# Kernel tuning notes

Hardware: AMD Instinct MI355X
Metric: run time of the kernel (lower is better)

Reference implementation:

```python
import jax, jax.numpy as jnp
import numpy as np

EPS = 1e-7  # keras backend epsilon
B, D_IN, H, L, DEPTH = 16384, 784, 512, 32, 2

def _lrelu(x):
    return jax.nn.leaky_relu(x, 0.3)  # tf.keras LeakyReLU default alpha

def _router(h, W1, b1, W2, b2, W3, b3):
    h = _lrelu(h @ W1 + b1)
    h = _lrelu(h @ W2 + b2)
    return jax.nn.sigmoid((h @ W3 + b3)[:, 0])

def setup_inputs():
    key = jax.random.key(0)
    ks = jax.random.split(key, 20)
    s = 0.02
    n = lambda k, sh: jax.random.normal(k, sh, jnp.float32) * s
    return {
        'x': jax.random.uniform(ks[0], (B, D_IN), jnp.float32),
        'enc_W0': n(ks[1], (D_IN, H)), 'enc_b0': jnp.zeros((H,), jnp.float32),
        'enc_W': n(ks[2], (3, H, H)), 'enc_b': jnp.zeros((3, H), jnp.float32),
        'dense_Wmu': n(ks[3], (7, H, L)), 'dense_bmu': jnp.zeros((7, L), jnp.float32),
        'dense_Wsig': n(ks[4], (7, H, L)), 'dense_bsig': jnp.zeros((7, L), jnp.float32),
        'trans_Wh': n(ks[5], (6, L, H)), 'trans_bh': jnp.zeros((6, H), jnp.float32),
        'trans_Wmu': n(ks[6], (6, H, L)), 'trans_bmu': jnp.zeros((6, L), jnp.float32),
        'trans_Wsig': n(ks[7], (6, H, L)), 'trans_bsig': jnp.zeros((6, L), jnp.float32),
        'routp_W1': n(ks[8], (3, L, H)), 'routp_b1': jnp.zeros((3, H), jnp.float32),
        'routp_W2': n(ks[9], (3, H, H)), 'routp_b2': jnp.zeros((3, H), jnp.float32),
        'routp_W3': n(ks[10], (3, H, 1)), 'routp_b3': jnp.zeros((3, 1), jnp.float32),
        'routq_W1': n(ks[11], (3, H, H)), 'routq_b1': jnp.zeros((3, H), jnp.float32),
        'routq_W2': n(ks[12], (3, H, H)), 'routq_b2': jnp.zeros((3, H), jnp.float32),
        'routq_W3': n(ks[13], (3, H, 1)), 'routq_b3': jnp.zeros((3, 1), jnp.float32),
        'dec_W1': n(ks[14], (4, L, H)), 'dec_b1': jnp.zeros((4, H), jnp.float32),
        'dec_W2': n(ks[15], (4, H, D_IN)), 'dec_b2': jnp.zeros((4, D_IN), jnp.float32),
    }

def reference(x, enc_W0, enc_b0, enc_W, enc_b,
              dense_Wmu, dense_bmu, dense_Wsig, dense_bsig,
              trans_Wh, trans_bh, trans_Wmu, trans_bmu, trans_Wsig, trans_bsig,
              routp_W1, routp_b1, routp_W2, routp_b2, routp_W3, routp_b3,
              routq_W1, routq_b1, routq_W2, routq_b2, routq_W3, routq_b3,
              dec_W1, dec_b1, dec_W2, dec_b2):
    Bn = x.shape[0]
    # bottom-up encoder chain; encoders collects layers i >= len - (depth+1) = 1
    d = _lrelu(x @ enc_W0 + enc_b0)
    encoders = []
    for i in range(3):
        d = _lrelu(d @ enc_W[i] + enc_b[i])
        encoders.append(d)
    depth_of = [0, 1, 1, 2, 2, 2, 2]  # BFS depth of the 7 tree nodes
    probs = {0: jnp.ones((Bn,), x.dtype)}
    zs = {}
    kl_nodes_tot = jnp.zeros((Bn,), x.dtype)
    kl_dec_tot = jnp.zeros((Bn,), x.dtype)
    kl_root = None
    leaves_prob, recons = [], []
    base = jax.random.key(1)
    for k in range(7):
        dl = depth_of[k]
        d = encoders[DEPTH - dl]
        mu_q_hat = d @ dense_Wmu[k] + dense_bmu[k]
        sig_q_hat = jax.nn.softplus(d @ dense_Wsig[k] + dense_bsig[k])
        if k == 0:
            mu_p = jnp.zeros_like(mu_q_hat)
            sig_p = jnp.ones_like(sig_q_hat)
            mu_q, sig_q = mu_q_hat, sig_q_hat
        else:
            zp = zs[(k - 1) // 2]
            h = _lrelu(zp @ trans_Wh[k - 1] + trans_bh[k - 1])
            mu_p = h @ trans_Wmu[k - 1] + trans_bmu[k - 1]
            sig_p = jax.nn.softplus(h @ trans_Wsig[k - 1] + trans_bsig[k - 1])
            # compute_posterior: precision-weighted fusion
            sig_q = 1.0 / (1.0 / sig_q_hat + 1.0 / sig_p)
            mu_q = sig_q * (mu_q_hat / sig_q_hat + mu_p / sig_p)
        vq = sig_q + EPS
        vp = sig_p + EPS
        # KL(N(mu_q, vq) || N(mu_p, vp)) for diag Gaussians (scale = sqrt(sigma+eps))
        kl = 0.5 * jnp.sum(vq / vp + (mu_q - mu_p) ** 2 / vp - 1.0 + jnp.log(vp / vq), axis=1)
        kl_node = jnp.clip(probs[k] * kl, -1.0, 1000.0)
        if k == 0:
            kl_root = kl_node
        else:
            kl_nodes_tot = kl_nodes_tot + kl_node
        eps_n = jax.random.normal(jax.random.fold_in(base, k), mu_q.shape, x.dtype)
        z = mu_q + jnp.sqrt(vq) * eps_n  # reparameterized sample
        zs[k] = z
        if k < 3:  # internal node: routing
            pl = _router(z, routp_W1[k], routp_b1[k], routp_W2[k], routp_b2[k], routp_W3[k], routp_b3[k])
            plq = _router(d, routq_W1[k], routq_b1[k], routq_W2[k], routq_b2[k], routq_W3[k], routq_b3[k])
            kl_dec = plq * jnp.log(EPS + plq / (pl + EPS)) + (1.0 - plq) * jnp.log(EPS + (1.0 - plq) / (1.0 - pl + EPS))
            kl_dec_tot = kl_dec_tot + probs[k] * kl_dec
            probs[2 * k + 1] = probs[k] * plq
            probs[2 * k + 2] = probs[k] * (1.0 - plq)
        else:  # leaf: decode
            leaves_prob.append(probs[k])
            h = _lrelu(z @ dec_W1[k - 3] + dec_b1[k - 3])
            recons.append(jax.nn.sigmoid(h @ dec_W2[k - 3] + dec_b2[k - 3]))
    rec_losses = jnp.zeros((Bn,), x.dtype)
    for p, r in zip(leaves_prob, recons):
        bce = -jnp.sum(x * jnp.log(r + EPS) + (1.0 - x) * jnp.log(1.0 - r + EPS), axis=1)
        rec_losses = rec_losses + p * bce
    # elbo_samples, per-sample total loss (shape [B])
    return kl_nodes_tot + kl_dec_tot + kl_root + rec_losses
```

## Files before the change

### kernel.cpp

```cpp
#include <hip/hip_runtime.h>
#include <cstdint>
#include <cstddef>

#define B_ROWS 16384
#define DIN 784
#define HD 512
#define LD 32

typedef __attribute__((ext_vector_type(8))) short short8;
typedef __attribute__((ext_vector_type(4))) float f32x4;
typedef __attribute__((ext_vector_type(4))) unsigned short us4;

struct I4 { int x, y, z, w; };
__device__ inline int i4get(I4 v, int z) { return z == 0 ? v.x : z == 1 ? v.y : z == 2 ? v.z : v.w; }

__device__ inline unsigned short f2bf(float v) {
  union { float f; unsigned u; } x; x.f = v;
  unsigned r = x.u + 0x7fffu + ((x.u >> 16) & 1u);
  return (unsigned short)(r >> 16);
}

__host__ __device__ inline void threefry2x32(uint32_t k0, uint32_t k1,
                                             uint32_t x0, uint32_t x1,
                                             uint32_t& o0, uint32_t& o1) {
  uint32_t ks2 = k0 ^ k1 ^ 0x1BD11BDAu;
#define TF_ROT(x, d) (((x) << (d)) | ((x) >> (32 - (d))))
#define TF_R(r) { x0 += x1; x1 = TF_ROT(x1, r); x1 ^= x0; }
  x0 += k0; x1 += k1;
  TF_R(13) TF_R(15) TF_R(26) TF_R(6)
  x0 += k1; x1 += ks2 + 1u;
  TF_R(17) TF_R(29) TF_R(16) TF_R(24)
  x0 += ks2; x1 += k0 + 2u;
  TF_R(13) TF_R(15) TF_R(26) TF_R(6)
  x0 += k0; x1 += k1 + 3u;
  TF_R(17) TF_R(29) TF_R(16) TF_R(24)
  x0 += k1; x1 += ks2 + 4u;
  TF_R(13) TF_R(15) TF_R(26) TF_R(6)
  x0 += ks2; x1 += k0 + 5u;
  o0 = x0; o1 = x1;
#undef TF_R
#undef TF_ROT
}

__device__ inline float erfinv_f(float x) {
  float w = -log1pf(-x * x);
  float p;
  if (w < 5.0f) {
    w -= 2.5f;
    p = 2.81022636e-08f;
    p = fmaf(p, w, 3.43273939e-07f);
    p = fmaf(p, w, -3.5233877e-06f);
    p = fmaf(p, w, -4.39150654e-06f);
    p = fmaf(p, w, 0.00021858087f);
    p = fmaf(p, w, -0.00125372503f);
    p = fmaf(p, w, -0.00417768164f);
    p = fmaf(p, w, 0.246640727f);
    p = fmaf(p, w, 1.50140941f);
  } else {
    w = sqrtf(w) - 3.0f;
    p = -0.000200214257f;
    p = fmaf(p, w, 0.000100950558f);
    p = fmaf(p, w, 0.00134934322f);
    p = fmaf(p, w, -0.00367342844f);
    p = fmaf(p, w, 0.00573950773f);
    p = fmaf(p, w, -0.0076224613f);
    p = fmaf(p, w, 0.00943887047f);
    p = fmaf(p, w, 1.00167406f);
    p = fmaf(p, w, 2.83297682f);
  }
  return p * x;
}

__device__ inline float jax_normal_elem(uint32_t ka, uint32_t kb, uint32_t idx) {
  uint32_t b1, b2;
  threefry2x32(ka, kb, 0u, idx, b1, b2);
  uint32_t bits = b1 ^ b2;
  uint32_t fb = (bits >> 9) | 0x3f800000u;
  float f = __uint_as_float(fb) - 1.0f;
  const float lo = -0.99999994f;
  float u = f * 2.0f + lo;
  u = fmaxf(u, lo);
  return 1.41421356f * erfinv_f(u);
}

struct WJob {
  unsigned short pi;
  unsigned src_off, dst_off, start;
  short K, N, Np, Kp;
};
struct WJobs { WJob j[56]; unsigned total; };

constexpr WJobs make_jobs() {
  WJobs W{};
  int idx = 0; unsigned start = 0; unsigned d = 0;
  auto add = [&](int pi, unsigned so, int K, int N, int Np, int Kp, unsigned doff) {
    W.j[idx].pi = (unsigned short)pi; W.j[idx].src_off = so; W.j[idx].dst_off = doff;
    W.j[idx].start = start; W.j[idx].K = (short)K; W.j[idx].N = (short)N;
    W.j[idx].Np = (short)Np; W.j[idx].Kp = (short)Kp;
    start += (unsigned)(Np * Kp); ++idx;
  };
  add(0, 0, 784, 512, 512, 800, d); d += 512 * 800;
  for (int i = 0; i < 3; ++i) { add(1, i * 262144u, 512, 512, 512, 512, d); d += 262144; }
  for (int k = 0; k < 7; ++k) { add(2, k * 16384u, 512, 32, 32, 512, d);
                                add(3, k * 16384u, 512, 32, 32, 512, d + 16384); d += 32768; }
  for (int i = 0; i < 6; ++i) { add(4, i * 16384u, 32, 512, 512, 32, d); d += 16384; }
  for (int i = 0; i < 6; ++i) { add(5, i * 16384u, 512, 32, 32, 512, d);
                                add(6, i * 16384u, 512, 32, 32, 512, d + 16384); d += 32768; }
  for (int k = 0; k < 3; ++k) { add(7, k * 16384u, 32, 512, 512, 32, d); d += 16384; }
  for (int k = 0; k < 3; ++k) { add(8, k * 262144u, 512, 512, 512, 512, d); d += 262144; }
  for (int k = 0; k < 3; ++k) { add(9, k * 262144u, 512, 512, 512, 512, d); d += 262144; }
  for (int k = 0; k < 3; ++k) { add(10, k * 262144u, 512, 512, 512, 512, d); d += 262144; }
  for (int i = 0; i < 4; ++i) { add(11, i * 16384u, 32, 512, 512, 32, d); d += 16384; }
  for (int i = 0; i < 4; ++i) { add(12, i * 401408u, 512, 784, 896, 512, d); d += 458752; }
  W.total = start;
  return W;
}
__device__ constexpr WJobs g_jobs = make_jobs();

struct TileTable { unsigned ts[57]; };
constexpr TileTable make_tiles() {
  TileTable T{}; WJobs J = make_jobs();
  unsigned acc = 0;
  for (int i = 0; i < 56; ++i) {
    T.ts[i] = acc;
    acc += (unsigned)(J.j[i].Np / 32) * (unsigned)(J.j[i].Kp / 32);
  }
  T.ts[56] = acc;
  return T;
}
__device__ constexpr TileTable g_tiles = make_tiles();

#define OFF_ENC0T 0u
#define OFF_ENCT 409600u
#define OFF_DENSE 1196032u
#define OFF_TWH 1425408u
#define OFF_TMS 1523712u
#define OFF_RP1 1720320u
#define OFF_RP2 1769472u
#define OFF_RQ1 2555904u
#define OFF_RQ2 3342336u
#define OFF_DC1 4128768u
#define OFF_DC2 4194304u
#define ARENA_ELEMS 6029312u

struct WSrcs { const float* p[13]; };

__global__ void wconv_k(WSrcs srcs, unsigned short* __restrict__ arena) {
  __shared__ unsigned short tile[32][34];
  unsigned bid = blockIdx.x;
  int jo = 0;
#pragma unroll 1
  while (jo + 1 < 56 && g_tiles.ts[jo + 1] <= bid) ++jo;
  const WJob J = g_jobs.j[jo];
  unsigned t = bid - g_tiles.ts[jo];
  unsigned ktiles = (unsigned)J.Kp / 32u;
  unsigned n0 = (t / ktiles) * 32u, k0 = (t % ktiles) * 32u;
  int ty = threadIdx.x >> 3, tx4 = (threadIdx.x & 7) * 4;
  float v0 = 0, v1 = 0, v2 = 0, v3 = 0;
  int kk = (int)k0 + ty;
  if (kk < J.K) {
    const float* sp = srcs.p[J.pi] + J.src_off + (size_t)kk * J.N + n0 + tx4;
    int nb = (int)(n0 + tx4);
    if (nb + 3 < J.N) {
      float4 v = *reinterpret_cast<const float4*>(sp);
      v0 = v.x; v1 = v.y; v2 = v.z; v3 = v.w;
    } else {
      if (nb + 0 < J.N) v0 = sp[0];
      if (nb + 1 < J.N) v1 = sp[1];
      if (nb + 2 < J.N) v2 = sp[2];
      if (nb + 3 < J.N) v3 = sp[3];
    }
  }
  tile[tx4 + 0][ty] = f2bf(v0);
  tile[tx4 + 1][ty] = f2bf(v1);
  tile[tx4 + 2][ty] = f2bf(v2);
  tile[tx4 + 3][ty] = f2bf(v3);
  __syncthreads();
  us4 w;
  w.x = tile[ty][tx4 + 0]; w.y = tile[ty][tx4 + 1];
  w.z = tile[ty][tx4 + 2]; w.w = tile[ty][tx4 + 3];
  *reinterpret_cast<us4*>(&arena[J.dst_off + (size_t)(n0 + ty) * J.Kp + k0 + tx4]) = w;
}

__global__ void xconv_k(const float* __restrict__ x, unsigned short* __restrict__ xb) {
  unsigned g = blockIdx.x * 256u + threadIdx.x;
  unsigned r = g / 200u, c4 = g % 200u;
  unsigned c = c4 * 4u;
  float v0 = 0, v1 = 0, v2 = 0, v3 = 0;
  if (c + 3 < 784u) {
    float4 v = *reinterpret_cast<const float4*>(x + (size_t)r * 784u + c);
    v0 = v.x; v1 = v.y; v2 = v.z; v3 = v.w;
  } else {
    if (c + 0 < 784u) v0 = x[(size_t)r * 784u + c + 0];
    if (c + 1 < 784u) v1 = x[(size_t)r * 784u + c + 1];
    if (c + 2 < 784u) v2 = x[(size_t)r * 784u + c + 2];
    if (c + 3 < 784u) v3 = x[(size_t)r * 784u + c + 3];
  }
  us4 w; w.x = f2bf(v0); w.y = f2bf(v1); w.z = f2bf(v2); w.w = f2bf(v3);
  *reinterpret_cast<us4*>(&xb[(size_t)r * 800u + c]) = w;
}

template <int BN, int ACT, typename OT>
__global__ void mgemm_k(const unsigned short* __restrict__ A, int sA,
                        const unsigned short* __restrict__ Wt,
                        const float* __restrict__ b1, const float* __restrict__ b2,
                        OT* __restrict__ C, int sC, int Nreal, int K,
                        I4 zAo, I4 zWo, I4 zCo, int zB1, int zB2,
                        const float* __restrict__ xx) {
  constexpr int BM = 128, BK = 32;
  constexpr int WN = BN / 2;
  constexpr int NF = WN / 16;
  __shared__ unsigned short As[BM][BK];
  __shared__ unsigned short Bs[BN][BK];
  __shared__ float sums[BM][2];
  const int z = blockIdx.z;
  A += i4get(zAo, z);
  Wt += i4get(zWo, z);
  C += i4get(zCo, z);
  b1 += (size_t)z * zB1;
  if (ACT == 3 || ACT == 4) { if (b2) b2 += (size_t)z * zB2; }

  const int tid = threadIdx.x;
  const int lane = tid & 63;
  const int wid = tid >> 6;
  const int wr = wid >> 1, wc = wid & 1;
  const int bm = blockIdx.x * BM;
  const int bn = blockIdx.y * BN;

  f32x4 acc[4][NF];
#pragma unroll
  for (int m = 0; m < 4; ++m)
#pragma unroll
    for (int n = 0; n < NF; ++n) acc[m][n] = (f32x4){0.f, 0.f, 0.f, 0.f};

  const int lr = lane >> 2;
  const int lk = (lane & 3) * 8;

  for (int k0 = 0; k0 < K; k0 += BK) {
#pragma unroll
    for (int cc = 0; cc < 2; ++cc) {
      int c = wid * 2 + cc;
      const unsigned short* g = A + (size_t)(bm + c * 16 + lr) * sA + k0 + lk;
      __builtin_amdgcn_global_load_lds(
          (const __attribute__((address_space(1))) void*)g,
          (__attribute__((address_space(3))) void*)(&As[c * 16][0]), 16, 0, 0);
    }
    constexpr int CB = BN / 16;
#pragma unroll
    for (int cc = 0; cc < CB / 4; ++cc) {
      int c = wid * (CB / 4) + cc;
      const unsigned short* g = Wt + (size_t)(bn + c * 16 + lr) * K + k0 + lk;
      __builtin_amdgcn_global_load_lds(
          (const __attribute__((address_space(1))) void*)g,
          (__attribute__((address_space(3))) void*)(&Bs[c * 16][0]), 16, 0, 0);
    }
    __syncthreads();

    short8 aF[4], bF[NF];
    const int ar = wr * 64 + (lane & 15);
    const int ac = (lane >> 4) * 8;
#pragma unroll
    for (int m = 0; m < 4; ++m)
      aF[m] = *reinterpret_cast<const short8*>(&As[ar + m * 16][ac]);
    const int br = wc * WN + (lane & 15);
#pragma unroll
    for (int n = 0; n < NF; ++n)
      bF[n] = *reinterpret_cast<const short8*>(&Bs[br + n * 16][ac]);
#pragma unroll
    for (int m = 0; m < 4; ++m)
#pragma unroll
      for (int n = 0; n < NF; ++n)
        acc[m][n] = __builtin_amdgcn_mfma_f32_16x16x32_bf16(aF[m], bF[n], acc[m][n], 0, 0, 0);
    __syncthreads();
  }

  if constexpr (ACT == 4 || ACT == 5) {
    const int row0 = bm + wr * 64 + (lane >> 4) * 4;
#pragma unroll
    for (int m = 0; m < 4; ++m) {
#pragma unroll
      for (int r = 0; r < 4; ++r) {
        float s = 0.0f;
        int grow = row0 + m * 16 + r;
#pragma unroll
        for (int n = 0; n < NF; ++n) {
          int col = bn + wc * WN + n * 16 + (lane & 15);
          float v = acc[m][n][r];
          if constexpr (ACT == 4) {
            v += b1[col];
            v = (v >= 0.0f) ? v : 0.3f * v;
            s += v * b2[col];
          } else {
            if (col < Nreal) {
              v += b1[col];
              float sg = 1.0f / (1.0f + expf(-v));
              float xv = xx[(size_t)grow * Nreal + col];
              s += xv * logf(sg + 1e-7f) + (1.0f - xv) * logf(1.0f - sg + 1e-7f);
            }
          }
        }
#pragma unroll
        for (int msk = 1; msk < 16; msk <<= 1) s += __shfl_xor(s, msk, 64);
        if ((lane & 15) == 0) sums[wr * 64 + m * 16 + (lane >> 4) * 4 + r][wc] = s;
      }
    }
    __syncthreads();
    if (tid < BM) {
      float* Cf = (float*)C;
      Cf[(size_t)(bm + tid) * sC + blockIdx.y] = sums[tid][0] + sums[tid][1];
    }
  } else {
#pragma unroll
    for (int m = 0; m < 4; ++m) {
      int row = bm + wr * 64 + m * 16 + (lane >> 4) * 4;
#pragma unroll
      for (int n = 0; n < NF; ++n) {
        int col = bn + wc * WN + n * 16 + (lane & 15);
        if (col < Nreal) {
#pragma unroll
          for (int r = 0; r < 4; ++r) {
            float v = acc[m][n][r];
            if constexpr (ACT == 3) {
              int nl = col >> 6, cin = col & 63;
              if (cin < 32) {
                v += b1[nl * 32 + cin];
              } else {
                v += b2[nl * 32 + (cin - 32)];
                v = fmaxf(v, 0.0f) + log1pf(expf(-fabsf(v)));
              }
            } else {
              v += b1[col];
              if (ACT == 1) v = (v >= 0.0f) ? v : 0.3f * v;
            }
            size_t oidx = (size_t)(row + r) * sC + col;
            if constexpr (sizeof(OT) == 2) C[oidx] = (OT)f2bf(v);
            else C[oidx] = (OT)v;
          }
        }
      }
    }
  }
}

struct Keys { uint32_t a[7]; uint32_t b[7]; };

__global__ void node_k(int kstart, Keys keys,
                       const float* __restrict__ musigAll,
                       const float* __restrict__ mupsigAll,
                       const float* __restrict__ probs,
                       unsigned short* __restrict__ zbuf,
                       float* __restrict__ contrib) {
  const int knode = kstart + blockIdx.y;
  const int row = blockIdx.x * 8 + (threadIdx.x >> 5);
  const int j = threadIdx.x & 31;
  const float* mq = musigAll + (size_t)row * 448 + 64 * knode;
  float mqh = mq[j], sqh = mq[32 + j];
  float mu_q, sig_q, mu_p, sig_p;
  if (knode == 0) {
    mu_p = 0.0f; sig_p = 1.0f; mu_q = mqh; sig_q = sqh;
  } else {
    const float* mp = mupsigAll + (size_t)row * 448 + 64 * knode;
    mu_p = mp[j]; sig_p = mp[32 + j];
    sig_q = 1.0f / (1.0f / sqh + 1.0f / sig_p);
    mu_q = sig_q * (mqh / sqh + mu_p / sig_p);
  }
  float vq = sig_q + 1e-7f, vp = sig_p + 1e-7f;
  float dm = mu_q - mu_p;
  float kj = vq / vp + dm * dm / vp - 1.0f + logf(vp / vq);
#pragma unroll
  for (int msk = 1; msk < 32; msk <<= 1) kj += __shfl_xor(kj, msk, 64);
  float e = jax_normal_elem(keys.a[knode], keys.b[knode], (uint32_t)(row * 32 + j));
  zbuf[(size_t)knode * B_ROWS * 32 + (size_t)row * 32 + j] = f2bf(mu_q + sqrtf(vq) * e);
  if (j == 0) {
    float p = (knode == 0) ? 1.0f : probs[(size_t)knode * B_ROWS + row];
    float kn = fminf(fmaxf(p * 0.5f * kj, -1.0f), 1000.0f);
    contrib[(size_t)knode * B_ROWS + row] = kn;
  }
}

__global__ void route_k(int kstart, const float* __restrict__ plp,
                        const float* __restrict__ plqp,
                        const float* __restrict__ rpb3, const float* __restrict__ rqb3,
                        float* __restrict__ probs, float* __restrict__ contrib) {
  const int k = kstart + blockIdx.y;
  const int row = blockIdx.x * 256 + threadIdx.x;
  const float* pp = plp + ((size_t)k * B_ROWS + row) * 4;
  const float* pq = plqp + ((size_t)k * B_ROWS + row) * 4;
  float sl = pp[0] + pp[1] + pp[2] + pp[3];
  float sq = pq[0] + pq[1] + pq[2] + pq[3];
  float pl = 1.0f / (1.0f + expf(-(sl + rpb3[k])));
  float plq = 1.0f / (1.0f + expf(-(sq + rqb3[k])));
  float p = (k == 0) ? 1.0f : probs[(size_t)k * B_ROWS + row];
  float kld = plq * logf(1e-7f + plq / (pl + 1e-7f)) +
              (1.0f - plq) * logf(1e-7f + (1.0f - plq) / (1.0f - pl + 1e-7f));
  contrib[(size_t)(7 + k) * B_ROWS + row] = p * kld;
  probs[(size_t)(2 * k + 1) * B_ROWS + row] = p * plq;
  probs[(size_t)(2 * k + 2) * B_ROWS + row] = p * (1.0f - plq);
}

__global__ void final_k(const float* __restrict__ contrib, const float* __restrict__ probs,
                        const float* __restrict__ pbce, float* __restrict__ out) {
  const int row = blockIdx.x * 256 + threadIdx.x;
  float s = 0.0f;
#pragma unroll
  for (int i = 0; i < 10; ++i) s += contrib[(size_t)i * B_ROWS + row];
#pragma unroll
  for (int l = 0; l < 4; ++l) {
    const float* pb = pbce + ((size_t)l * B_ROWS + row) * 7;
    float bs = 0.0f;
#pragma unroll
    for (int y = 0; y < 7; ++y) bs += pb[y];
    s += probs[(size_t)(3 + l) * B_ROWS + row] * (-bs);
  }
  out[row] = s;
}

extern "C" void kernel_launch(void* const* d_in, const int* in_sizes, int n_in,
                              void* d_out, int out_size, void* d_ws, size_t ws_size,
                              hipStream_t stream) {
  const float* x      = (const float*)d_in[0];
  const float* enc_W0 = (const float*)d_in[1];
  const float* enc_b0 = (const float*)d_in[2];
  const float* enc_W  = (const float*)d_in[3];
  const float* enc_b  = (const float*)d_in[4];
  const float* dWmu   = (const float*)d_in[5];
  const float* dbmu   = (const float*)d_in[6];
  const float* dWsig  = (const float*)d_in[7];
  const float* dbsig  = (const float*)d_in[8];
  const float* tWh    = (const float*)d_in[9];
  const float* tbh    = (const float*)d_in[10];
  const float* tWmu   = (const float*)d_in[11];
  const float* tbmu   = (const float*)d_in[12];
  const float* tWsig  = (const float*)d_in[13];
  const float* tbsig  = (const float*)d_in[14];
  const float* rpW1   = (const float*)d_in[15];
  const float* rpb1   = (const float*)d_in[16];
  const float* rpW2   = (const float*)d_in[17];
  const float* rpb2   = (const float*)d_in[18];
  const float* rpW3   = (const float*)d_in[19];
  const float* rpb3   = (const float*)d_in[20];
  const float* rqW1   = (const float*)d_in[21];
  const float* rqb1   = (const float*)d_in[22];
  const float* rqW2   = (const float*)d_in[23];
  const float* rqb2   = (const float*)d_in[24];
  const float* rqW3   = (const float*)d_in[25];
  const float* rqb3   = (const float*)d_in[26];
  const float* dcW1   = (const float*)d_in[27];
  const float* dcb1   = (const float*)d_in[28];
  const float* dcW2   = (const float*)d_in[29];
  const float* dcb2   = (const float*)d_in[30];
  float* out = (float*)d_out;
  (void)in_sizes; (void)n_in; (void)out_size; (void)ws_size;

  const size_t BR = B_ROWS;
  unsigned short* h = (unsigned short*)d_ws;
  unsigned short* bufH = h;
  unsigned short* encA = h + BR * 512;
  unsigned short* encB = h + BR * 1024;
  unsigned short* encC = h + BR * 1536;
  unsigned short* bufT = h + BR * 2048;
  unsigned short* zbuf = h + BR * 3072;
  unsigned short* arena = h + BR * 3296;
  size_t ho = BR * 3296 + ARENA_ELEMS;
  float* f = (float*)(h + ho);
  float* musigAll  = f;
  float* mupsigAll = f + BR * 448;
  float* probs     = f + BR * 896;
  float* plp       = f + BR * 903;
  float* plqp      = f + BR * 915;
  float* pbce      = f + BR * 927;
  float* contrib   = f + BR * 955;
  unsigned short* xb = (unsigned short*)f;

  const int offA = (int)(BR * 512);
  const int offC = (int)(BR * 1536);

  Keys keys;
  for (int k = 0; k < 7; ++k) threefry2x32(0u, 1u, 0u, (uint32_t)k, keys.a[k], keys.b[k]);

  const I4 Z0 = {0, 0, 0, 0};
  constexpr TileTable HT = make_tiles();

  xconv_k<<<dim3((B_ROWS * 200) / 256), 256, 0, stream>>>(x, xb);
  WSrcs srcs;
  srcs.p[0] = enc_W0; srcs.p[1] = enc_W; srcs.p[2] = dWmu; srcs.p[3] = dWsig;
  srcs.p[4] = tWh; srcs.p[5] = tWmu; srcs.p[6] = tWsig;
  srcs.p[7] = rpW1; srcs.p[8] = rpW2; srcs.p[9] = rqW1; srcs.p[10] = rqW2;
  srcs.p[11] = dcW1; srcs.p[12] = dcW2;
  wconv_k<<<dim3(HT.ts[56]), 256, 0, stream>>>(srcs, arena);

#define LAUNCH(BN, ACT, OT, A, sA, W, B1, B2, Cc, sC, Nr, K, gy, gz, zA, zW, zC, zb1, zb2, XX) \
  mgemm_k<BN, ACT, OT><<<dim3(B_ROWS / 128, gy, gz), 256, 0, stream>>>( \
      A, sA, W, B1, B2, Cc, sC, Nr, K, zA, zW, zC, zb1, zb2, XX)

  LAUNCH(128, 1, unsigned short, xb, 800, arena + OFF_ENC0T, enc_b0, nullptr,
         bufH, 512, 512, 800, 4, 1, Z0, Z0, Z0, 0, 0, nullptr);
  LAUNCH(128, 1, unsigned short, bufH, 512, arena + OFF_ENCT + 0u, enc_b + 0, nullptr,
         encA, 512, 512, 512, 4, 1, Z0, Z0, Z0, 0, 0, nullptr);
  LAUNCH(128, 3, float, encA, 512, arena + OFF_DENSE + 3u * 32768u, dbmu + 96, dbsig + 96,
         musigAll + 192, 448, 256, 512, 2, 1, Z0, Z0, Z0, 0, 0, nullptr);
  LAUNCH(128, 1, unsigned short, encA, 512, arena + OFF_ENCT + 262144u, enc_b + 512, nullptr,
         encB, 512, 512, 512, 4, 1, Z0, Z0, Z0, 0, 0, nullptr);
  LAUNCH(128, 3, float, encB, 512, arena + OFF_DENSE + 32768u, dbmu + 32, dbsig + 32,
         musigAll + 64, 448, 128, 512, 1, 1, Z0, Z0, Z0, 0, 0, nullptr);
  LAUNCH(128, 1, unsigned short, encB, 512, arena + OFF_ENCT + 524288u, enc_b + 1024, nullptr,
         encC, 512, 512, 512, 4, 1, Z0, Z0, Z0, 0, 0, nullptr);
  LAUNCH(64, 3, float, encC, 512, arena + OFF_DENSE, dbmu, dbsig,
         musigAll, 448, 64, 512, 1, 1, Z0, Z0, Z0, 0, 0, nullptr);
  LAUNCH(128, 1, unsigned short, encC, 512, arena + OFF_RQ1, rqb1, nullptr,
         bufH, 512, 512, 512, 4, 1, Z0, Z0, Z0, 0, 0, nullptr);
  {
    I4 zW = {0, 262144, 0, 0}, zC = {offA, offC, 0, 0};
    LAUNCH(128, 1, unsigned short, encB, 512, arena + OFF_RQ1 + 262144u, rqb1 + 512, nullptr,
           h, 512, 512, 512, 4, 2, Z0, zW, zC, 512, 0, nullptr);
  }
  {
    I4 zA = {0, offA, offC, 0};
    I4 zW = {0, 262144, 524288, 0};
    I4 zC = {0, (int)(BR * 4), (int)(BR * 8), 0};
    LAUNCH(128, 4, float, h, 512, arena + OFF_RQ2, rqb2, rqW3,
           plqp, 4, 512, 512, 4, 3, zA, zW, zC, 512, 512, nullptr);
  }

  node_k<<<dim3(B_ROWS / 8, 1), 256, 0, stream>>>(0, keys, musigAll, mupsigAll, probs, zbuf, contrib);
  LAUNCH(128, 1, unsigned short, zbuf, 32, arena + OFF_RP1, rpb1, nullptr,
         bufT, 512, 512, 32, 4, 1, Z0, Z0, Z0, 0, 0, nullptr);
  LAUNCH(128, 4, float, bufT, 512, arena + OFF_RP2, rpb2, rpW3,
         plp, 4, 512, 512, 4, 1, Z0, Z0, Z0, 0, 0, nullptr);
  route_k<<<dim3(B_ROWS / 256, 1), 256, 0, stream>>>(0, plp, plqp, rpb3, rqb3, probs, contrib);

  LAUNCH(128, 1, unsigned short, zbuf, 32, arena + OFF_TWH, tbh, nullptr,
         bufT, 1024, 1024, 32, 8, 1, Z0, Z0, Z0, 0, 0, nullptr);
  {
    I4 zA = {0, 512, 0, 0}, zW = {0, 32768, 0, 0}, zC = {0, 64, 0, 0};
    LAUNCH(64, 3, float, bufT, 1024, arena + OFF_TMS, tbmu, tbsig,
           mupsigAll + 64, 448, 64, 512, 1, 2, zA, zW, zC, 32, 32, nullptr);
  }
  node_k<<<dim3(B_ROWS / 8, 2), 256, 0, stream>>>(1, keys, musigAll, mupsigAll, probs, zbuf, contrib);
  {
    I4 zA = {0, (int)(BR * 32), 0, 0}, zW = {0, 16384, 0, 0}, zC = {offA, offC, 0, 0};
    LAUNCH(128, 1, unsigned short, zbuf + BR * 32, 32, arena + OFF_RP1 + 16384u, rpb1 + 512, nullptr,
           h, 512, 512, 32, 4, 2, zA, zW, zC, 512, 0, nullptr);
    I4 zA2 = {offA, offC, 0, 0}, zW2 = {0, 262144, 0, 0}, zC2 = {0, (int)(BR * 4), 0, 0};
    LAUNCH(128, 4, float, h, 512, arena + OFF_RP2 + 262144u, rpb2 + 512, rpW3 + 512,
           plp + BR * 4, 4, 512, 512, 4, 2, zA2, zW2, zC2, 512, 512, nullptr);
  }
  route_k<<<dim3(B_ROWS / 256, 2), 256, 0, stream>>>(1, plp, plqp, rpb3, rqb3, probs, contrib);

  {
    I4 zA = {0, 512, 0, 0}, zW = {0, 32768, 0, 0}, zC = {0, 64, 0, 0};
    LAUNCH(128, 1, unsigned short, zbuf + BR * 32, 32, arena + OFF_TWH + 32768u, tbh + 1024, nullptr,
           bufT, 1024, 1024, 32, 8, 1, Z0, Z0, Z0, 0, 0, nullptr);
    LAUNCH(64, 3, float, bufT, 1024, arena + OFF_TMS + 65536u, tbmu + 64, tbsig + 64,
           mupsigAll + 192, 448, 64, 512, 1, 2, zA, zW, zC, 32, 32, nullptr);
    LAUNCH(128, 1, unsigned short, zbuf + BR * 64, 32, arena + OFF_TWH + 65536u, tbh + 2048, nullptr,
           bufT, 1024, 1024, 32, 8, 1, Z0, Z0, Z0, 0, 0, nullptr);
    LAUNCH(64, 3, float, bufT, 1024, arena + OFF_TMS + 131072u, tbmu + 128, tbsig + 128,
           mupsigAll + 320, 448, 64, 512, 1, 2, zA, zW, zC, 32, 32, nullptr);
  }
  node_k<<<dim3(B_ROWS / 8, 4), 256, 0, stream>>>(3, keys, musigAll, mupsigAll, probs, zbuf, contrib);

  {
    I4 zA1 = {0, (int)(BR * 32), 0, 0}, zW1 = {0, 16384, 0, 0}, zC1 = {0, (int)(BR * 512), 0, 0};
    I4 zA2 = {0, (int)(BR * 512), 0, 0}, zW2 = {0, 458752, 0, 0}, zC2 = {0, (int)(BR * 7), 0, 0};
    LAUNCH(128, 1, unsigned short, zbuf + BR * 96, 32, arena + OFF_DC1, dcb1, nullptr,
           bufT, 512, 512, 32, 4, 2, zA1, zW1, zC1, 512, 0, nullptr);
    LAUNCH(128, 5, float, bufT, 512, arena + OFF_DC2, dcb2, nullptr,
           pbce, 7, 784, 512, 7, 2, zA2, zW2, zC2, 784, 0, x);
    LAUNCH(128, 1, unsigned short, zbuf + BR * 160, 32, arena + OFF_DC1 + 32768u, dcb1 + 1024, nullptr,
           bufT, 512, 512, 32, 4, 2, zA1, zW1, zC1, 512, 0, nullptr);
    LAUNCH(128, 5, float, bufT, 512, arena + OFF_DC2 + 917504u, dcb2 + 1568, nullptr,
           pbce + BR * 14, 7, 784, 512, 7, 2, zA2, zW2, zC2, 784, 0, x);
  }

  final_k<<<dim3(B_ROWS / 256), 256, 0, stream>>>(contrib, probs, pbce, out);
#undef LAUNCH
}
```

Before: 687.2 us.

## Double-buffer GEMM LDS tiles and read BCE targets from bf16 copy of x

The MFMA GEMM kernel now double-buffers its A and B shared-memory tiles, issuing the global-to-LDS loads for the next K step before computing the current one, so memory latency can overlap with compute and one barrier per iteration is dropped. The xconv kernel also writes a compact 784-wide bf16 copy of x, which the fused decoder BCE epilogue reads in place of fp32 x, halving that traffic. Workspace buffers are reshuffled so the extra copy fits. This doubles LDS use per block, which may lower occupancy, and rounding x to bf16 slightly changes the loss values.

Measured after the change: 690.3 us. No clear change (+0.4%).

```diff
diff --git a/kernel.cpp b/kernel.cpp
--- a/kernel.cpp
+++ b/kernel.cpp
@@ -18,6 +18,10 @@
   union { float f; unsigned u; } x; x.f = v;
   unsigned r = x.u + 0x7fffu + ((x.u >> 16) & 1u);
   return (unsigned short)(r >> 16);
+}
+__device__ inline float bf2f(unsigned short b) {
+  union { unsigned u; float f; } x; x.u = ((unsigned)b) << 16;
+  return x.f;
 }
 
 __host__ __device__ inline void threefry2x32(uint32_t k0, uint32_t k1,
@@ -182,7 +186,8 @@
   *reinterpret_cast<us4*>(&arena[J.dst_off + (size_t)(n0 + ty) * J.Kp + k0 + tx4]) = w;
 }
 
-__global__ void xconv_k(const float* __restrict__ x, unsigned short* __restrict__ xb) {
+__global__ void xconv_k(const float* __restrict__ x, unsigned short* __restrict__ xb800,
+                        unsigned short* __restrict__ xb784) {
   unsigned g = blockIdx.x * 256u + threadIdx.x;
   unsigned r = g / 200u, c4 = g % 200u;
   unsigned c = c4 * 4u;
@@ -197,7 +202,9 @@
     if (c + 3 < 784u) v3 = x[(size_t)r * 784u + c + 3];
   }
   us4 w; w.x = f2bf(v0); w.y = f2bf(v1); w.z = f2bf(v2); w.w = f2bf(v3);
-  *reinterpret_cast<us4*>(&xb[(size_t)r * 800u + c]) = w;
+  *reinterpret_cast<us4*>(&xb800[(size_t)r * 800u + c]) = w;
+  if (c + 3 < 784u)
+    *reinterpret_cast<us4*>(&xb784[(size_t)r * 784u + c]) = w;
 }
 
 template <int BN, int ACT, typename OT>
@@ -206,12 +213,12 @@
                         const float* __restrict__ b1, const float* __restrict__ b2,
                         OT* __restrict__ C, int sC, int Nreal, int K,
                         I4 zAo, I4 zWo, I4 zCo, int zB1, int zB2,
-                        const float* __restrict__ xx) {
+                        const unsigned short* __restrict__ xx) {
   constexpr int BM = 128, BK = 32;
   constexpr int WN = BN / 2;
   constexpr int NF = WN / 16;
-  __shared__ unsigned short As[BM][BK];
-  __shared__ unsigned short Bs[BN][BK];
+  __shared__ unsigned short As[2][BM][BK];
+  __shared__ unsigned short Bs[2][BN][BK];
   __shared__ float sums[BM][2];
   const int z = blockIdx.z;
   A += i4get(zAo, z);
@@ -226,24 +233,17 @@
   const int wr = wid >> 1, wc = wid & 1;
   const int bm = blockIdx.x * BM;
   const int bn = blockIdx.y * BN;
-
-  f32x4 acc[4][NF];
-#pragma unroll
-  for (int m = 0; m < 4; ++m)
-#pragma unroll
-    for (int n = 0; n < NF; ++n) acc[m][n] = (f32x4){0.f, 0.f, 0.f, 0.f};
-
   const int lr = lane >> 2;
   const int lk = (lane & 3) * 8;
 
-  for (int k0 = 0; k0 < K; k0 += BK) {
+  auto stage = [&](int buf, int k0) {
 #pragma unroll
     for (int cc = 0; cc < 2; ++cc) {
       int c = wid * 2 + cc;
       const unsigned short* g = A + (size_t)(bm + c * 16 + lr) * sA + k0 + lk;
       __builtin_amdgcn_global_load_lds(
           (const __attribute__((address_space(1))) void*)g,
-          (__attribute__((address_space(3))) void*)(&As[c * 16][0]), 16, 0, 0);
+          (__attribute__((address_space(3))) void*)(&As[buf][c * 16][0]), 16, 0, 0);
     }
     constexpr int CB = BN / 16;
 #pragma unroll
@@ -252,20 +252,34 @@
       const unsigned short* g = Wt + (size_t)(bn + c * 16 + lr) * K + k0 + lk;
       __builtin_amdgcn_global_load_lds(
           (const __attribute__((address_space(1))) void*)g,
-          (__attribute__((address_space(3))) void*)(&Bs[c * 16][0]), 16, 0, 0);
+          (__attribute__((address_space(3))) void*)(&Bs[buf][c * 16][0]), 16, 0, 0);
     }
-    __syncthreads();
+  };
+
+  f32x4 acc[4][NF];
+#pragma unroll
+  for (int m = 0; m < 4; ++m)
+#pragma unroll
+    for (int n = 0; n < NF; ++n) acc[m][n] = (f32x4){0.f, 0.f, 0.f, 0.f};
+
+  stage(0, 0);
+  __syncthreads();
+
+  const int nt = K / BK;
+  for (int t = 0; t < nt; ++t) {
+    const int cur = t & 1;
+    if (t + 1 < nt) stage(cur ^ 1, (t + 1) * BK);
 
     short8 aF[4], bF[NF];
     const int ar = wr * 64 + (lane & 15);
     const int ac = (lane >> 4) * 8;
 #pragma unroll
     for (int m = 0; m < 4; ++m)
-      aF[m] = *reinterpret_cast<const short8*>(&As[ar + m * 16][ac]);
+      aF[m] = *reinterpret_cast<const short8*>(&As[cur][ar + m * 16][ac]);
     const int br = wc * WN + (lane & 15);
 #pragma unroll
     for (int n = 0; n < NF; ++n)
-      bF[n] = *reinterpret_cast<const short8*>(&Bs[br + n * 16][ac]);
+      bF[n] = *reinterpret_cast<const short8*>(&Bs[cur][br + n * 16][ac]);
 #pragma unroll
     for (int m = 0; m < 4; ++m)
 #pragma unroll
@@ -294,7 +308,7 @@
             if (col < Nreal) {
               v += b1[col];
               float sg = 1.0f / (1.0f + expf(-v));
-              float xv = xx[(size_t)grow * Nreal + col];
+              float xv = bf2f(xx[(size_t)grow * Nreal + col]);
               s += xv * logf(sg + 1e-7f) + (1.0f - xv) * logf(1.0f - sg + 1e-7f);
             }
           }
@@ -454,14 +468,14 @@
 
   const size_t BR = B_ROWS;
   unsigned short* h = (unsigned short*)d_ws;
-  unsigned short* bufH = h;
-  unsigned short* encA = h + BR * 512;
-  unsigned short* encB = h + BR * 1024;
-  unsigned short* encC = h + BR * 1536;
-  unsigned short* bufT = h + BR * 2048;
-  unsigned short* zbuf = h + BR * 3072;
-  unsigned short* arena = h + BR * 3296;
-  size_t ho = BR * 3296 + ARENA_ELEMS;
+  unsigned short* encA  = h;
+  unsigned short* encB  = h + BR * 512;
+  unsigned short* encC  = h + BR * 1024;
+  unsigned short* bufT  = h + BR * 1536;
+  unsigned short* zbuf  = h + BR * 2560;
+  unsigned short* xb784 = h + BR * 2784;
+  unsigned short* arena = h + BR * 3568;
+  size_t ho = BR * 3568 + ARENA_ELEMS;
   float* f = (float*)(h + ho);
   float* musigAll  = f;
   float* mupsigAll = f + BR * 448;
@@ -470,10 +484,11 @@
   float* plqp      = f + BR * 915;
   float* pbce      = f + BR * 927;
   float* contrib   = f + BR * 955;
-  unsigned short* xb = (unsigned short*)f;
-
-  const int offA = (int)(BR * 512);
-  const int offC = (int)(BR * 1536);
+  unsigned short* xb800 = (unsigned short*)f;
+
+  const int offA = 0;
+  const int offC = (int)(BR * 1024);
+  const int offT = (int)(BR * 1536);
 
   Keys keys;
   for (int k = 0; k < 7; ++k) threefry2x32(0u, 1u, 0u, (uint32_t)k, keys.a[k], keys.b[k]);
@@ -481,7 +496,7 @@
   const I4 Z0 = {0, 0, 0, 0};
   constexpr TileTable HT = make_tiles();
 
-  xconv_k<<<dim3((B_ROWS * 200) / 256), 256, 0, stream>>>(x, xb);
+  xconv_k<<<dim3((B_ROWS * 200) / 256), 256, 0, stream>>>(x, xb800, xb784);
   WSrcs srcs;
   srcs.p[0] = enc_W0; srcs.p[1] = enc_W; srcs.p[2] = dWmu; srcs.p[3] = dWsig;
   srcs.p[4] = tWh; srcs.p[5] = tWmu; srcs.p[6] = tWsig;
@@ -493,9 +508,9 @@
   mgemm_k<BN, ACT, OT><<<dim3(B_ROWS / 128, gy, gz), 256, 0, stream>>>( \
       A, sA, W, B1, B2, Cc, sC, Nr, K, zA, zW, zC, zb1, zb2, XX)
 
-  LAUNCH(128, 1, unsigned short, xb, 800, arena + OFF_ENC0T, enc_b0, nullptr,
-         bufH, 512, 512, 800, 4, 1, Z0, Z0, Z0, 0, 0, nullptr);
-  LAUNCH(128, 1, unsigned short, bufH, 512, arena + OFF_ENCT + 0u, enc_b + 0, nullptr,
+  LAUNCH(128, 1, unsigned short, xb800, 800, arena + OFF_ENC0T, enc_b0, nullptr,
+         bufT, 512, 512, 800, 4, 1, Z0, Z0, Z0, 0, 0, nullptr);
+  LAUNCH(128, 1, unsigned short, bufT, 512, arena + OFF_ENCT + 0u, enc_b + 0, nullptr,
          encA, 512, 512, 512, 4, 1, Z0, Z0, Z0, 0, 0, nullptr);
   LAUNCH(128, 3, float, encA, 512, arena + OFF_DENSE + 3u * 32768u, dbmu + 96, dbsig + 96,
          musigAll + 192, 448, 256, 512, 2, 1, Z0, Z0, Z0, 0, 0, nullptr);
@@ -508,14 +523,14 @@
   LAUNCH(64, 3, float, encC, 512, arena + OFF_DENSE, dbmu, dbsig,
          musigAll, 448, 64, 512, 1, 1, Z0, Z0, Z0, 0, 0, nullptr);
   LAUNCH(128, 1, unsigned short, encC, 512, arena + OFF_RQ1, rqb1, nullptr,
-         bufH, 512, 512, 512, 4, 1, Z0, Z0, Z0, 0, 0, nullptr);
+         bufT, 512, 512, 512, 4, 1, Z0, Z0, Z0, 0, 0, nullptr);
   {
     I4 zW = {0, 262144, 0, 0}, zC = {offA, offC, 0, 0};
     LAUNCH(128, 1, unsigned short, encB, 512, arena + OFF_RQ1 + 262144u, rqb1 + 512, nullptr,
            h, 512, 512, 512, 4, 2, Z0, zW, zC, 512, 0, nullptr);
   }
   {
-    I4 zA = {0, offA, offC, 0};
+    I4 zA = {offT, offA, offC, 0};
     I4 zW = {0, 262144, 524288, 0};
     I4 zC = {0, (int)(BR * 4), (int)(BR * 8), 0};
     LAUNCH(128, 4, float, h, 512, arena + OFF_RQ2, rqb2, rqW3,
@@ -566,11 +581,11 @@
     LAUNCH(128, 1, unsigned short, zbuf + BR * 96, 32, arena + OFF_DC1, dcb1, nullptr,
            bufT, 512, 512, 32, 4, 2, zA1, zW1, zC1, 512, 0, nullptr);
     LAUNCH(128, 5, float, bufT, 512, arena + OFF_DC2, dcb2, nullptr,
-           pbce, 7, 784, 512, 7, 2, zA2, zW2, zC2, 784, 0, x);
+           pbce, 7, 784, 512, 7, 2, zA2, zW2, zC2, 784, 0, xb784);
     LAUNCH(128, 1, unsigned short, zbuf + BR * 160, 32, arena + OFF_DC1 + 32768u, dcb1 + 1024, nullptr,
            bufT, 512, 512, 32, 4, 2, zA1, zW1, zC1, 512, 0, nullptr);
     LAUNCH(128, 5, float, bufT, 512, arena + OFF_DC2 + 917504u, dcb2 + 1568, nullptr,
-           pbce + BR * 14, 7, 784, 512, 7, 2, zA2, zW2, zC2, 784, 0, x);
+           pbce + BR * 14, 7, 784, 512, 7, 2, zA2, zW2, zC2, 784, 0, xb784);
   }
 
   final_k<<<dim3(B_ROWS / 256), 256, 0, stream>>>(contrib, probs, pbce, out);
```
